# Kernel tuning notes

Hardware: AMD Instinct MI355X
Metric: run time of the kernel (lower is better)

## Reference

```python
import jax, jax.numpy as jnp
import numpy as np

EPS = 1e-20
TEMP = 0.07
HEAD_DIM = 128


def setup_inputs() -> dict:
    key = jax.random.key(0)
    k1, k2, k3 = jax.random.split(key, 3)
    B, C, T, H, W = 4, 512, 8, 32, 32
    x = jax.random.normal(k1, (B, C, T, H, W), dtype=jnp.float32)
    W_head = jax.random.normal(k2, (C, HEAD_DIM), dtype=jnp.float32) / np.sqrt(C).astype(np.float32)
    b_head = jax.random.normal(k3, (HEAD_DIM,), dtype=jnp.float32) * 0.01
    return {"x": x, "W_head": W_head, "b_head": b_head}


def _forward(x, W_head, b_head):
    B, C, T, H, W = x.shape
    N = H * W
    # linear head over channel dim (equivalent to permute->Linear->permute)
    feats = jnp.einsum('bcthw,cd->bdthw', x, W_head) + b_head[None, :, None, None, None]
    keys = feats.reshape(B, HEAD_DIM, T, N)
    # F.normalize(p=2, dim=1): x / max(||x||, 1e-12)
    norm = jnp.maximum(jnp.linalg.norm(keys, axis=1, keepdims=True), 1e-12)
    keys = keys / norm
    # affinity between consecutive frames: [B, T-1, N, N]
    A = jnp.einsum('bctn,bctm->btnm', keys[:, :, :-1], keys[:, :, 1:])
    A12 = jax.nn.softmax(A / TEMP, axis=-1)                         # forward stochastic mats
    A21 = jax.nn.softmax(jnp.swapaxes(A, -1, -2) / TEMP, axis=-1)   # backward stochastic mats
    A12s = jnp.swapaxes(A12, 0, 1)  # [T-1, B, N, N]
    A21s = jnp.swapaxes(A21, 0, 1)  # [T-1, B, N, N]

    # prefix products P[i] = A12[0] @ A12[1] @ ... @ A12[i]
    def step_p(carry, a):
        c = carry @ a
        return c, c
    _, Ptail = jax.lax.scan(step_p, A12s[0], A12s[1:])
    P = jnp.concatenate([A12s[:1], Ptail], axis=0)  # [T-1, B, N, N]

    # suffix products S[i] = A21[i] @ A21[i-1] @ ... @ A21[0]
    def step_s(carry, a):
        c = a @ carry
        return c, c
    _, Stail = jax.lax.scan(step_s, A21s[0], A21s[1:])
    S = jnp.concatenate([A21s[:1], Stail], axis=0)  # [T-1, B, N, N]

    # cycle walks for i = 1..T-2: aar_i = P[i] @ S[i]
    aars = jnp.matmul(P[1:], S[1:])  # [T-2, B, N, N]
    logits = jnp.log(aars + EPS)
    # cross-entropy with identity targets: loss = logsumexp - logit[n, n]
    lse = jax.nn.logsumexp(logits, axis=-1)                  # [T-2, B, N]
    diag = jnp.diagonal(logits, axis1=-2, axis2=-1)          # [T-2, B, N]
    losses = jnp.mean(lse - diag, axis=(1, 2))               # [T-2]
    preds = jnp.argmax(logits, axis=-1)                      # [T-2, B, N]
    tgt = jnp.arange(N)[None, None, :]
    accs = jnp.mean((preds == tgt).astype(jnp.float32), axis=(1, 2))
    # original returns (loss_of_last_walk, diags); diags exposed as stacked arrays
    return losses[-1], losses, accs


def reference(x, W_head, b_head):
    return _forward(x, W_head, b_head)
```

## Files before the change

### kernel.cpp

```cpp
#include <hip/hip_runtime.h>
#include <cstdint>
#include <cstddef>

typedef unsigned short u16;
typedef unsigned long long u64;
using short8 = __attribute__((ext_vector_type(8))) short;
using f32x4  = __attribute__((ext_vector_type(4))) float;

#define KEXP 20.609929155556620f

__device__ __forceinline__ u16 f2bf(float f) {
  unsigned u = __float_as_uint(f);
  u += 0x7fffu + ((u >> 16) & 1u);
  return (u16)(u >> 16);
}
__device__ __forceinline__ float bf2f(u16 h) { return __uint_as_float(((unsigned)h) << 16); }

typedef const unsigned int GASu32 __attribute__((address_space(1)));
typedef unsigned int LASu32 __attribute__((address_space(3)));

__device__ __forceinline__ void gload16(const u16* src, u16* dstLds) {
  __builtin_amdgcn_global_load_lds((GASu32*)src, (LASu32*)dstLds, 16, 0, 0);
}

__global__ __launch_bounds__(256) void transpose_x(const float* __restrict__ x, u16* __restrict__ xT) {
  __shared__ float t[32][33];
  int b = blockIdx.z, c0 = blockIdx.y * 32, s0 = blockIdx.x * 32;
  int tid = threadIdx.x;
  int ci = tid >> 3, s4 = (tid & 7) * 4;
  float4 v = *(const float4*)(x + ((size_t)b * 512 + c0 + ci) * 8192 + s0 + s4);
  t[ci][s4 + 0] = v.x; t[ci][s4 + 1] = v.y; t[ci][s4 + 2] = v.z; t[ci][s4 + 3] = v.w;
  __syncthreads();
  int si = tid >> 3, c4 = (tid & 7) * 4;
  ushort4 o;
  o.x = f2bf(t[c4 + 0][si]); o.y = f2bf(t[c4 + 1][si]);
  o.z = f2bf(t[c4 + 2][si]); o.w = f2bf(t[c4 + 3][si]);
  *(ushort4*)(xT + ((size_t)b * 8192 + s0 + si) * 512 + c0 + c4) = o;
}

__global__ __launch_bounds__(256) void transpose_w(const float* __restrict__ W, u16* __restrict__ Wt) {
  int idx = blockIdx.x * 256 + threadIdx.x;
  int d = idx >> 9, c = idx & 511;
  Wt[idx] = f2bf(W[c * 128 + d]);
}

__global__ __launch_bounds__(256) void normalize_keys(u16* __restrict__ keys) {
  int wv = threadIdx.x >> 6, lane = threadIdx.x & 63;
  int row = blockIdx.x * 4 + wv;
  unsigned* p = (unsigned*)(keys + (size_t)row * 128) + lane;
  unsigned v = *p;
  float a = bf2f((u16)(v & 0xffffu)), b = bf2f((u16)(v >> 16));
  float s = a * a + b * b;
  #pragma unroll
  for (int m = 1; m < 64; m <<= 1) s += __shfl_xor(s, m, 64);
  float sc = 1.f / fmaxf(sqrtf(s), 1e-12f);
  *p = (unsigned)f2bf(a * sc) | ((unsigned)f2bf(b * sc) << 16);
}

__global__ __launch_bounds__(256) void k3_t0(const u16* __restrict__ E, const float* __restrict__ rsum,
                                             const float* __restrict__ csum,
                                             u16* __restrict__ P0, u16* __restrict__ S0) {
  int b = blockIdx.z, r = blockIdx.x;
  int zE = b * 7;
  const u16* e = E + ((size_t)zE << 20) + (size_t)r * 1024;
  float rr = 1.f / rsum[zE * 1024 + r];
  int c = threadIdx.x * 4;
  ushort4 v = *(const ushort4*)(e + c);
  float4 cv = *(const float4*)(csum + zE * 1024 + c);
  ushort4 o1, o2;
  float v0 = bf2f(v.x), v1 = bf2f(v.y), v2 = bf2f(v.z), v3 = bf2f(v.w);
  o1.x = f2bf(v0 * rr); o1.y = f2bf(v1 * rr); o1.z = f2bf(v2 * rr); o1.w = f2bf(v3 * rr);
  o2.x = f2bf(v0 / cv.x); o2.y = f2bf(v1 / cv.y); o2.z = f2bf(v2 / cv.z); o2.w = f2bf(v3 / cv.w);
  size_t base = ((size_t)b << 20) + (size_t)r * 1024 + c;
  *(ushort4*)(P0 + base) = o1;
  *(ushort4*)(S0 + base) = o2;
}

__global__ __launch_bounds__(256) void k3_tr(const u16* __restrict__ E, const float* __restrict__ rsum,
                                             const float* __restrict__ csum,
                                             u16* __restrict__ Bp, u16* __restrict__ Bs) {
  __shared__ u16 t[64][66];
  int z = blockIdx.z; int b = z / 6, tt = z % 6 + 1;
  int zE = b * 7 + tt;
  int er0 = blockIdx.x * 64, ec0 = blockIdx.y * 64;
  const u16* e = E + ((size_t)zE << 20);
  int tid = threadIdx.x;
  int ri = tid >> 4, c4 = (tid & 15) * 4;
  #pragma unroll
  for (int p = 0; p < 4; ++p) {
    ushort4 v = *(const ushort4*)(e + (size_t)(er0 + ri + p * 16) * 1024 + ec0 + c4);
    t[ri + p * 16][c4 + 0] = v.x; t[ri + p * 16][c4 + 1] = v.y;
    t[ri + p * 16][c4 + 2] = v.z; t[ri + p * 16][c4 + 3] = v.w;
  }
  __syncthreads();
  size_t outBase = (size_t)(b * 6 + tt - 1) << 20;
  float ir0 = 1.f / rsum[zE * 1024 + er0 + c4 + 0];
  float ir1 = 1.f / rsum[zE * 1024 + er0 + c4 + 1];
  float ir2 = 1.f / rsum[zE * 1024 + er0 + c4 + 2];
  float ir3 = 1.f / rsum[zE * 1024 + er0 + c4 + 3];
  #pragma unroll
  for (int p = 0; p < 4; ++p) {
    int roL = ri + p * 16;
    int ro = ec0 + roL;
    float ic = 1.f / csum[zE * 1024 + ro];
    float v0 = bf2f(t[c4 + 0][roL]), v1 = bf2f(t[c4 + 1][roL]);
    float v2 = bf2f(t[c4 + 2][roL]), v3 = bf2f(t[c4 + 3][roL]);
    ushort4 op, os;
    op.x = f2bf(v0 * ir0); op.y = f2bf(v1 * ir1); op.z = f2bf(v2 * ir2); op.w = f2bf(v3 * ir3);
    os.x = f2bf(v0 * ic);  os.y = f2bf(v1 * ic);  os.z = f2bf(v2 * ic);  os.w = f2bf(v3 * ic);
    size_t off = outBase + (size_t)ro * 1024 + er0 + c4;
    *(ushort4*)(Bp + off) = op;
    *(ushort4*)(Bs + off) = os;
  }
}

struct GemmBatch { const u16* A[24]; const u16* B[24]; u16* C[8]; };
enum { M_HEAD = 0, M_EXP = 1, M_PLAIN = 2, M_AAR = 3 };

__device__ __forceinline__ void stage_tile(const u16* __restrict__ g, int ld, int r0, int k0, u16* lds) {
  int tid = threadIdx.x;
  int lane = tid & 63, wv = tid >> 6;
  #pragma unroll
  for (int j = 0; j < 4; ++j) {
    int gi = ((wv << 2) + j) * 64 + lane;
    int row = gi >> 3;
    int wp = (gi & 7) << 4;
    int lc = wp ^ ((row & 7) << 4);
    const u16* src = g + (size_t)(r0 + row) * ld + k0 + (lc >> 1);
    gload16(src, lds + ((wv << 2) + j) * 512);
  }
}

__device__ __forceinline__ short8 frag_ld(const u16* s, int row, int kb) {
  int off = row * 128 + (kb ^ ((row & 7) << 4));
  return *(const short8*)((const char*)s + off);
}

template <int MODE>
__global__ __launch_bounds__(256) void gemm_nt(const u16* __restrict__ gA, const u16* __restrict__ gB,
                                               u16* __restrict__ gC, GemmBatch batch,
                                               const float* __restrict__ bias,
                                               float* __restrict__ rowsumR, u64* __restrict__ amax,
                                               float* __restrict__ diagv,
                                               float* __restrict__ rsumE, float* __restrict__ csumE) {
  __shared__ u16 As[2][128 * 64];
  __shared__ u16 Bs[2][128 * 64];
  int tid = threadIdx.x, lane = tid & 63, wv = tid >> 6;
  int wr = wv >> 1, wc = wv & 1;
  int z = blockIdx.z;
  const u16 *A, *B; u16* C;
  int K, lda, ldb, ldc;
  if constexpr (MODE == M_HEAD) {
    A = gA; B = gB; C = gC; K = 512; lda = 512; ldb = 512; ldc = 128;
  } else if constexpr (MODE == M_EXP) {
    int b = z / 7, t = z % 7;
    size_t offA = (size_t)(b * 8 + t) * 131072;
    A = gA + offA; B = gA + offA + 131072; C = gC + ((size_t)z << 20);
    K = 128; lda = 128; ldb = 128; ldc = 1024;
  } else if constexpr (MODE == M_PLAIN) {
    A = batch.A[z]; B = batch.B[z]; C = batch.C[z];
    K = 1024; lda = 1024; ldb = 1024; ldc = 1024;
  } else {
    A = batch.A[z]; B = batch.B[z]; C = nullptr;
    K = 1024; lda = 1024; ldb = 1024; ldc = 1024;
  }
  int m0 = blockIdx.x * 128, n0 = blockIdx.y * 128;

  f32x4 acc[4][4] = {};
  int nt = K >> 6;

  stage_tile(A, lda, m0, 0, As[0]);
  stage_tile(B, ldb, n0, 0, Bs[0]);
  __syncthreads();

  for (int kt = 0; kt < nt; ++kt) {
    int cur = kt & 1;
    if (kt + 1 < nt) {
      stage_tile(A, lda, m0, (kt + 1) << 6, As[cur ^ 1]);
      stage_tile(B, ldb, n0, (kt + 1) << 6, Bs[cur ^ 1]);
    }
    const u16* Ac = As[cur];
    const u16* Bc = Bs[cur];
    #pragma unroll
    for (int ks = 0; ks < 2; ++ks) {
      short8 af[4], bfv[4];
      #pragma unroll
      for (int f = 0; f < 4; ++f) {
        af[f]  = frag_ld(Ac, (wr << 6) + (f << 4) + (lane & 15), (ks << 6) + ((lane >> 4) << 4));
        bfv[f] = frag_ld(Bc, (wc << 6) + (f << 4) + (lane & 15), (ks << 6) + ((lane >> 4) << 4));
      }
      #pragma unroll
      for (int fr = 0; fr < 4; ++fr)
        #pragma unroll
        for (int fc = 0; fc < 4; ++fc)
          acc[fr][fc] = __builtin_amdgcn_mfma_f32_16x16x32_bf16(af[fr], bfv[fc], acc[fr][fc], 0, 0, 0);
    }
    __syncthreads();
  }

  if constexpr (MODE == M_AAR) {
    #pragma unroll
    for (int fr = 0; fr < 4; ++fr) {
      #pragma unroll
      for (int j = 0; j < 4; ++j) {
        float rs = 0.f, mv = -1.f; int mc = 0;
        #pragma unroll
        for (int fc = 0; fc < 4; ++fc) {
          float v = acc[fr][fc][j];
          rs += v;
          int c = n0 + (wc << 6) + (fc << 4) + (lane & 15);
          if (v > mv) { mv = v; mc = c; }
        }
        u64 pk = ((u64)__float_as_uint(mv) << 32) | (u64)(unsigned)(1023 - mc);
        #pragma unroll
        for (int m = 1; m < 16; m <<= 1) {
          rs += __shfl_xor(rs, m, 64);
          u64 o = __shfl_xor(pk, m, 64);
          pk = (o > pk) ? o : pk;
        }
        if ((lane & 15) == 0) {
          int row = m0 + (wr << 6) + (fr << 4) + ((lane >> 4) << 2) + j;
          atomicAdd(&rowsumR[(z << 10) + row], rs);
          atomicMax(&amax[(z << 10) + row], pk);
        }
      }
      if (m0 == n0 && wr == wc) {
        int jj = (lane & 15) - ((lane >> 4) << 2);
        if (jj >= 0 && jj < 4) {
          int row = m0 + (wr << 6) + (fr << 4) + (lane & 15);
          float dv = (jj == 0) ? acc[fr][fr][0] : (jj == 1) ? acc[fr][fr][1]
                    : (jj == 2) ? acc[fr][fr][2] : acc[fr][fr][3];
          diagv[(z << 10) + row] = dv;
        }
      }
    }
  } else if constexpr (MODE == M_EXP) {
    float rp[4][4] = {};
    float cp[4] = {};
    #pragma unroll
    for (int fr = 0; fr < 4; ++fr)
      #pragma unroll
      for (int fc = 0; fc < 4; ++fc)
        #pragma unroll
        for (int j = 0; j < 4; ++j) {
          int row = m0 + (wr << 6) + (fr << 4) + ((lane >> 4) << 2) + j;
          int col = n0 + (wc << 6) + (fc << 4) + (lane & 15);
          float v = exp2f(acc[fr][fc][j] * KEXP);
          C[(size_t)row * ldc + col] = f2bf(v);
          rp[fr][j] += v;
          cp[fc] += v;
        }
    #pragma unroll
    for (int fr = 0; fr < 4; ++fr)
      #pragma unroll
      for (int j = 0; j < 4; ++j) {
        float r = rp[fr][j];
        r += __shfl_xor(r, 1, 64); r += __shfl_xor(r, 2, 64);
        r += __shfl_xor(r, 4, 64); r += __shfl_xor(r, 8, 64);
        if ((lane & 15) == 0) {
          int row = m0 + (wr << 6) + (fr << 4) + ((lane >> 4) << 2) + j;
          atomicAdd(&rsumE[z * 1024 + row], r);
        }
      }
    #pragma unroll
    for (int fc = 0; fc < 4; ++fc) {
      float c = cp[fc];
      c += __shfl_xor(c, 16, 64); c += __shfl_xor(c, 32, 64);
      if ((lane >> 4) == 0) {
        int col = n0 + (wc << 6) + (fc << 4) + (lane & 15);
        atomicAdd(&csumE[z * 1024 + col], c);
      }
    }
  } else {
    #pragma unroll
    for (int fr = 0; fr < 4; ++fr)
      #pragma unroll
      for (int fc = 0; fc < 4; ++fc)
        #pragma unroll
        for (int j = 0; j < 4; ++j) {
          int row = m0 + (wr << 6) + (fr << 4) + ((lane >> 4) << 2) + j;
          int col = n0 + (wc << 6) + (fc << 4) + (lane & 15);
          float v = acc[fr][fc][j];
          if constexpr (MODE == M_HEAD) v += bias[col];
          C[(size_t)row * ldc + col] = f2bf(v);
        }
  }
}

__global__ __launch_bounds__(256) void finalize_k(const float* __restrict__ rowsumR, const u64* __restrict__ amax,
                                                  const float* __restrict__ diagv, float* __restrict__ out) {
  __shared__ float sl[256], sa[256];
  int w = blockIdx.x;
  int tid = threadIdx.x;
  float ls = 0.f, ac = 0.f;
  for (int idx = tid; idx < 4096; idx += 256) {
    int zi = (w << 12) + idx;
    int n = idx & 1023;
    float rs = rowsumR[zi];
    float dv = diagv[zi];
    ls += logf(rs + 1024.f * 1e-20f) - logf(dv + 1e-20f);
    unsigned pred = 1023u - (unsigned)(amax[zi] & 0xffffffffULL);
    ac += (pred == (unsigned)n) ? 1.f : 0.f;
  }
  sl[tid] = ls; sa[tid] = ac;
  __syncthreads();
  for (int s2 = 128; s2 > 0; s2 >>= 1) {
    if (tid < s2) { sl[tid] += sl[tid + s2]; sa[tid] += sa[tid + s2]; }
    __syncthreads();
  }
  if (tid == 0) {
    float loss = sl[0] / 4096.f, acv = sa[0] / 4096.f;
    out[1 + w] = loss;
    out[7 + w] = acv;
    if (w == 5) out[0] = loss;
  }
}

extern "C" void kernel_launch(void* const* d_in, const int* in_sizes, int n_in,
                              void* d_out, int out_size, void* d_ws, size_t ws_size,
                              hipStream_t stream) {
  (void)in_sizes; (void)n_in; (void)out_size; (void)ws_size;
  const float* x  = (const float*)d_in[0];
  const float* Wh = (const float*)d_in[1];
  const float* bh = (const float*)d_in[2];
  float* out = (float*)d_out;
  char* ws = (char*)d_ws;
  const size_t MB = 1ull << 20;

  u16* xT   = (u16*)(ws);
  u16* keys = (u16*)(ws + 32 * MB);
  u16* Wt   = (u16*)(ws + 40 * MB);
  float* rsumE   = (float*)(ws + 40 * MB + 128 * 1024);
  float* csumE   = (float*)(ws + 40 * MB + 240 * 1024);
  float* rowsumR = (float*)(ws + 40 * MB + 352 * 1024);
  u64*   amax    = (u64*)(ws + 40 * MB + 448 * 1024);
  float* diagv   = (float*)(ws + 40 * MB + 640 * 1024);
  u16* E    = (u16*)(ws + 41 * MB);
  u16* Bp   = (u16*)(ws + 113 * MB);
  u16* Bs   = (u16*)(ws + 161 * MB);

  u16* Pb[7] = { (u16*)(ws + 97 * MB), (u16*)(ws + 0 * MB), (u16*)(ws + 8 * MB),
                 (u16*)(ws + 16 * MB), (u16*)(ws + 24 * MB), (u16*)(ws + 41 * MB),
                 (u16*)(ws + 49 * MB) };
  u16* Sb[7] = { (u16*)(ws + 105 * MB), (u16*)(ws + 57 * MB), (u16*)(ws + 65 * MB),
                 (u16*)(ws + 73 * MB), (u16*)(ws + 81 * MB), (u16*)(ws + 89 * MB),
                 (u16*)(ws + 97 * MB) };

  GemmBatch empty{};

  transpose_x<<<dim3(256, 16, 4), 256, 0, stream>>>(x, xT);
  transpose_w<<<dim3(256), 256, 0, stream>>>(Wh, Wt);
  gemm_nt<M_HEAD><<<dim3(256, 1, 1), 256, 0, stream>>>(xT, Wt, keys, empty, bh,
                                                       nullptr, nullptr, nullptr, nullptr, nullptr);
  normalize_keys<<<dim3(8192), 256, 0, stream>>>(keys);
  (void)hipMemsetAsync(rsumE, 0, 512 * 1024, stream);
  gemm_nt<M_EXP><<<dim3(8, 8, 28), 256, 0, stream>>>(keys, nullptr, E, empty, nullptr,
                                                     nullptr, nullptr, nullptr, rsumE, csumE);
  k3_t0<<<dim3(1024, 1, 4), 256, 0, stream>>>(E, rsumE, csumE, Pb[0], Sb[0]);
  k3_tr<<<dim3(16, 16, 24), 256, 0, stream>>>(E, rsumE, csumE, Bp, Bs);

  for (int i = 1; i <= 6; ++i) {
    GemmBatch gb{};
    for (int b = 0; b < 4; ++b) {
      gb.A[b]     = Pb[i - 1] + (size_t)b * 1048576;
      gb.B[b]     = Bp + (size_t)(b * 6 + i - 1) * 1048576;
      gb.C[b]     = Pb[i] + (size_t)b * 1048576;
      gb.A[4 + b] = Sb[i - 1] + (size_t)b * 1048576;
      gb.B[4 + b] = Bs + (size_t)(b * 6 + i - 1) * 1048576;
      gb.C[4 + b] = Sb[i] + (size_t)b * 1048576;
    }
    gemm_nt<M_PLAIN><<<dim3(8, 8, 8), 256, 0, stream>>>(nullptr, nullptr, nullptr, gb, nullptr,
                                                        nullptr, nullptr, nullptr, nullptr, nullptr);
  }

  GemmBatch ga{};
  for (int i = 1; i <= 6; ++i)
    for (int b = 0; b < 4; ++b) {
      ga.A[(i - 1) * 4 + b] = Pb[i] + (size_t)b * 1048576;
      ga.B[(i - 1) * 4 + b] = Sb[i] + (size_t)b * 1048576;
    }
  gemm_nt<M_AAR><<<dim3(8, 8, 24), 256, 0, stream>>>(nullptr, nullptr, nullptr, ga, nullptr,
                                                     rowsumR, amax, diagv, nullptr, nullptr);
  finalize_k<<<dim3(6), 256, 0, stream>>>(rowsumR, amax, diagv, out);
}
```

Before: 382.4 us.

## Use triple-buffered K=32 LDS pipeline with explicit vmcnt waits in GEMM

```diff
diff --git a/kernel.cpp b/kernel.cpp
--- a/kernel.cpp
+++ b/kernel.cpp
@@ -117,23 +117,28 @@
 struct GemmBatch { const u16* A[24]; const u16* B[24]; u16* C[8]; };
 enum { M_HEAD = 0, M_EXP = 1, M_PLAIN = 2, M_AAR = 3 };
 
-__device__ __forceinline__ void stage_tile(const u16* __restrict__ g, int ld, int r0, int k0, u16* lds) {
+__device__ __forceinline__ int lds_off32(int r, int kbyte) {
+  int rp = r >> 1;
+  int sl = (((r & 1) << 2) | (kbyte >> 4)) ^ (rp & 7);
+  return rp * 128 + sl * 16;
+}
+
+__device__ __forceinline__ void stage_tile32(const u16* __restrict__ g, int ld, int r0, int k0, u16* lds) {
   int tid = threadIdx.x;
-  int lane = tid & 63, wv = tid >> 6;
   #pragma unroll
-  for (int j = 0; j < 4; ++j) {
-    int gi = ((wv << 2) + j) * 64 + lane;
-    int row = gi >> 3;
-    int wp = (gi & 7) << 4;
-    int lc = wp ^ ((row & 7) << 4);
-    const u16* src = g + (size_t)(r0 + row) * ld + k0 + (lc >> 1);
-    gload16(src, lds + ((wv << 2) + j) * 512);
-  }
-}
-
-__device__ __forceinline__ short8 frag_ld(const u16* s, int row, int kb) {
-  int off = row * 128 + (kb ^ ((row & 7) << 4));
-  return *(const short8*)((const char*)s + off);
+  for (int j = 0; j < 2; ++j) {
+    int gidx = j * 256 + tid;
+    int rp = gidx >> 3, slot = gidx & 7;
+    int sp = slot ^ (rp & 7);
+    int r = (rp << 1) | (sp >> 2);
+    int kb16 = sp & 3;
+    const u16* src = g + (size_t)(r0 + r) * ld + k0 + kb16 * 8;
+    gload16(src, lds + gidx * 8);
+  }
+}
+
+__device__ __forceinline__ short8 frag_ld32(const u16* s, int row, int kbyte) {
+  return *(const short8*)((const char*)s + lds_off32(row, kbyte));
 }
 
 template <int MODE>
@@ -143,8 +148,8 @@
                                                float* __restrict__ rowsumR, u64* __restrict__ amax,
                                                float* __restrict__ diagv,
                                                float* __restrict__ rsumE, float* __restrict__ csumE) {
-  __shared__ u16 As[2][128 * 64];
-  __shared__ u16 Bs[2][128 * 64];
+  __shared__ u16 As[3][4096];
+  __shared__ u16 Bs[3][4096];
   int tid = threadIdx.x, lane = tid & 63, wv = tid >> 6;
   int wr = wv >> 1, wc = wv & 1;
   int z = blockIdx.z;
@@ -167,35 +172,38 @@
   int m0 = blockIdx.x * 128, n0 = blockIdx.y * 128;
 
   f32x4 acc[4][4] = {};
-  int nt = K >> 6;
-
-  stage_tile(A, lda, m0, 0, As[0]);
-  stage_tile(B, ldb, n0, 0, Bs[0]);
-  __syncthreads();
-
-  for (int kt = 0; kt < nt; ++kt) {
-    int cur = kt & 1;
-    if (kt + 1 < nt) {
-      stage_tile(A, lda, m0, (kt + 1) << 6, As[cur ^ 1]);
-      stage_tile(B, ldb, n0, (kt + 1) << 6, Bs[cur ^ 1]);
-    }
-    const u16* Ac = As[cur];
-    const u16* Bc = Bs[cur];
-    #pragma unroll
-    for (int ks = 0; ks < 2; ++ks) {
-      short8 af[4], bfv[4];
-      #pragma unroll
-      for (int f = 0; f < 4; ++f) {
-        af[f]  = frag_ld(Ac, (wr << 6) + (f << 4) + (lane & 15), (ks << 6) + ((lane >> 4) << 4));
-        bfv[f] = frag_ld(Bc, (wc << 6) + (f << 4) + (lane & 15), (ks << 6) + ((lane >> 4) << 4));
-      }
-      #pragma unroll
-      for (int fr = 0; fr < 4; ++fr)
-        #pragma unroll
-        for (int fc = 0; fc < 4; ++fc)
-          acc[fr][fc] = __builtin_amdgcn_mfma_f32_16x16x32_bf16(af[fr], bfv[fc], acc[fr][fc], 0, 0, 0);
-    }
-    __syncthreads();
+  int nt = K >> 5;
+
+  stage_tile32(A, lda, m0, 0,  As[0]); stage_tile32(B, ldb, n0, 0,  Bs[0]);
+  stage_tile32(A, lda, m0, 32, As[1]); stage_tile32(B, ldb, n0, 32, Bs[1]);
+  stage_tile32(A, lda, m0, 64, As[2]); stage_tile32(B, ldb, n0, 64, Bs[2]);
+
+  for (int t = 0; t < nt; ++t) {
+    int rem = nt - 1 - t;
+    if (rem >= 2)      asm volatile("s_waitcnt vmcnt(8)" ::: "memory");
+    else if (rem == 1) asm volatile("s_waitcnt vmcnt(4)" ::: "memory");
+    else               asm volatile("s_waitcnt vmcnt(0)" ::: "memory");
+    __builtin_amdgcn_s_barrier();
+    __builtin_amdgcn_sched_barrier(0);
+    const u16* Ac = As[t % 3];
+    const u16* Bc = Bs[t % 3];
+    short8 af[4], bfv[4];
+    #pragma unroll
+    for (int f = 0; f < 4; ++f) {
+      af[f]  = frag_ld32(Ac, (wr << 6) + (f << 4) + (lane & 15), (lane >> 4) << 4);
+      bfv[f] = frag_ld32(Bc, (wc << 6) + (f << 4) + (lane & 15), (lane >> 4) << 4);
+    }
+    #pragma unroll
+    for (int fr = 0; fr < 4; ++fr)
+      #pragma unroll
+      for (int fc = 0; fc < 4; ++fc)
+        acc[fr][fc] = __builtin_amdgcn_mfma_f32_16x16x32_bf16(af[fr], bfv[fc], acc[fr][fc], 0, 0, 0);
+    __builtin_amdgcn_sched_barrier(0);
+    __builtin_amdgcn_s_barrier();
+    if (t + 3 < nt) {
+      stage_tile32(A, lda, m0, (t + 3) << 5, As[t % 3]);
+      stage_tile32(B, ldb, n0, (t + 3) << 5, Bs[t % 3]);
+    }
   }
 
   if constexpr (MODE == M_AAR) {
```

New measurement: 369.0 us. -3.5%, faster.
